# Kernel tuning notes

Hardware: AMD Instinct MI355X
Metric: run time of the kernel (lower is better)

Reference implementation:

```python
import jax, jax.numpy as jnp
import numpy as np

BN_EPS = 1e-5

# Binary activation with hardtanh STE semantics (forward: sign)
@jax.custom_vjp
def binary_act(x):
    return jnp.sign(x)

def _ba_fwd(x):
    return jnp.sign(x), x

def _ba_bwd(x, g):
    return (jnp.where(jnp.abs(x) > 1.0, 0.0, g),)

binary_act.defvjp(_ba_fwd, _ba_bwd)

# Binary weight quantizer (forward: sign, backward: identity STE)
@jax.custom_vjp
def binary_w(x):
    return jnp.sign(x)

def _bw_fwd(x):
    return jnp.sign(x), None

def _bw_bwd(_, g):
    return (g,)

binary_w.defvjp(_bw_fwd, _bw_bwd)


def setup_inputs() -> dict:
    key = jax.random.key(0)
    k1, k2, k3 = jax.random.split(key, 3)
    B, C_in, H, W_sp = 32, 256, 56, 56
    C_out, KH, KW = 256, 3, 3
    x = jax.random.normal(k1, (B, C_in, H, W_sp), dtype=jnp.float32)
    weight = jax.random.normal(k2, (C_out, C_in, KH, KW), dtype=jnp.float32) * 0.05
    bias = jax.random.normal(k3, (C_out,), dtype=jnp.float32) * 0.01
    gamma = jnp.ones((C_out,), dtype=jnp.float32)
    beta = jnp.zeros((C_out,), dtype=jnp.float32)
    return {"x": x, "weight": weight, "bias": bias, "gamma": gamma, "beta": beta}


def reference(x, weight, bias, gamma, beta):
    # --- activation binarization (A=2): sign ---
    xb = binary_act(x)
    # --- weight binarization (W=2): mean-center over in-channel dim, clamp, sign * alpha ---
    wc = weight - jnp.mean(weight, axis=1, keepdims=True)
    wc = jnp.clip(wc, -1.0, 1.0)
    alpha = jnp.mean(jnp.abs(wc), axis=(1, 2, 3), keepdims=True)  # per-output-channel scale
    wq = binary_w(wc) * alpha
    # --- conv2d, stride 1, padding 1 ---
    y = jax.lax.conv_general_dilated(
        xb, wq, window_strides=(1, 1), padding=((1, 1), (1, 1)),
        dimension_numbers=("NCHW", "OIHW", "NCHW"))
    y = y + bias[None, :, None, None]
    # --- BatchNorm2d (training-mode batch statistics, biased variance) ---
    mu = jnp.mean(y, axis=(0, 2, 3), keepdims=True)
    var = jnp.var(y, axis=(0, 2, 3), keepdims=True)
    y = (y - mu) * jax.lax.rsqrt(var + BN_EPS)
    y = y * gamma[None, :, None, None] + beta[None, :, None, None]
    # --- last_relu=1 ---
    y = jax.nn.relu(y)
    # --- last_bin=1 (A=2 -> binary activation) ---
    y = binary_act(y)
    return y
```

## Files before the change

kernel.cpp:

```cpp
#include <hip/hip_runtime.h>

typedef unsigned long long u64;
typedef int i32x4 __attribute__((ext_vector_type(4)));
typedef int i32x16 __attribute__((ext_vector_type(16)));
typedef short s16x8 __attribute__((ext_vector_type(8)));
typedef float f32x4 __attribute__((ext_vector_type(4)));

#define N_SP 3136
#define C_IN 256
#define C_OUT 256
#define BATCH 32
#define NBLK 1792
#define XROW 64
#define XPLANE (58 * XROW * 256)
#define XSIZE ((size_t)BATCH * XPLANE)
#define S16_OFF ((size_t)36 << 20)
#define S16_BYTES ((size_t)BATCH * C_OUT * N_SP * 2)

__global__ __launch_bounds__(256) void prep_weights(const float* __restrict__ w,
                                                    char* __restrict__ A_pack,
                                                    double* __restrict__ alpha) {
    const int o = blockIdx.x;
    const int i = threadIdx.x;
    const int lane = i & 63, wvid = i >> 6;
    __shared__ double part[4][9];
    __shared__ double part2[4];

    float wv[9];
    const float* wp = w + ((size_t)o * C_IN + i) * 9;
#pragma unroll
    for (int t = 0; t < 9; ++t) wv[t] = wp[t];

#pragma unroll
    for (int t = 0; t < 9; ++t) {
        double v = (double)wv[t];
#pragma unroll
        for (int off = 32; off > 0; off >>= 1) v += __shfl_down(v, off);
        if (lane == 0) part[wvid][t] = v;
    }
    __syncthreads();

    double asum = 0.0;
#pragma unroll
    for (int t = 0; t < 9; ++t) {
        double mean = (part[0][t] + part[1][t] + part[2][t] + part[3][t]) * (1.0 / 256.0);
        double wc = (double)wv[t] - mean;
        int idx16 = ((t * 8 + (i >> 5)) * 8 + (o >> 5)) * 64 + (((i >> 4) & 1) << 5) + (o & 31);
        A_pack[(size_t)idx16 * 16 + (i & 15)] = (char)(wc > 0.0 ? 1 : -1);
        double aw = fabs(wc);
        if (aw > 1.0) aw = 1.0;
        asum += aw;
    }
#pragma unroll
    for (int off = 32; off > 0; off >>= 1) asum += __shfl_down(asum, off);
    if (lane == 0) part2[wvid] = asum;
    __syncthreads();
    if (i == 0)
        alpha[o] = (part2[0] + part2[1] + part2[2] + part2[3]) * (1.0 / 2304.0);
}

__global__ __launch_bounds__(256) void sign_transpose(const float* __restrict__ x,
                                                      char* __restrict__ xsT) {
    const int sp0 = blockIdx.x * 64;
    const int b = blockIdx.y;
    const int lane = threadIdx.x & 63;
    const int wv = threadIdx.x >> 6;
    __shared__ char tile[64 * 272];

    {
        const int tidl = (blockIdx.y * 49 + blockIdx.x) * 256 + threadIdx.x;
        if (tidl < 294912) {
            const int bb = tidl / 9216;
            const int r = tidl - bb * 9216;
            int hp, wp, c16;
            if (r < 2048) {
                hp = (r >> 10) * 57;
                wp = (r >> 4) & 63;
                c16 = (r & 15) << 4;
            } else {
                int r2 = r - 2048;
                hp = 1 + (r2 >> 7);
                int q = r2 & 127;
                int wi = q >> 4;
                wp = (wi == 0) ? 0 : 56 + wi;
                c16 = (q & 15) << 4;
            }
            *(i32x4*)(xsT + (((size_t)(bb * 58 + hp) << 6) + wp) * 256 + c16) =
                (i32x4){0, 0, 0, 0};
        }
    }

    const float* xp = x + ((size_t)(b * 256 + (wv << 6))) * N_SP + sp0 + lane;
#pragma unroll
    for (int q = 0; q < 4; ++q) {
        unsigned d[4];
#pragma unroll
        for (int dd = 0; dd < 4; ++dd) {
            unsigned v = 0;
#pragma unroll
            for (int kk = 0; kk < 4; ++kk) {
                int ci_l = (q << 4) + (dd << 2) + kk;
                float xv = __builtin_nontemporal_load(xp + (size_t)ci_l * N_SP);
                v |= (unsigned)(xv > 0.0f ? 0x01u : 0xFFu) << (8 * kk);
            }
            d[dd] = v;
        }
        *(i32x4*)(tile + lane * 272 + (wv << 6) + (q << 4)) =
            (i32x4){(int)d[0], (int)d[1], (int)d[2], (int)d[3]};
    }
    __syncthreads();

    const int t = threadIdx.x;
#pragma unroll
    for (int j = 0; j < 4; ++j) {
        int sp_loc = (j << 4) + (t >> 4);
        int ci0 = (t & 15) << 4;
        i32x4 v = *(const i32x4*)(tile + sp_loc * 272 + ci0);
        int spg = sp0 + sp_loc;
        int h = spg / 56, w = spg - h * 56;
        size_t dst = (((size_t)(b * 58 + h + 1) << 6) + (w + 1)) * 256 + ci0;
        *(i32x4*)(xsT + dst) = v;
    }
}

__global__ __launch_bounds__(256, 3) void conv_mfma(const char* __restrict__ xsT,
                                                    const char* __restrict__ A_pack,
                                                    float* __restrict__ out,
                                                    short* __restrict__ s16,
                                                    int2* __restrict__ partials) {
    const int tid = threadIdx.x;
    const int lane = tid & 63;
    const int wv = tid >> 6;
    const int l31 = lane & 31, l5 = lane >> 5;
    const int blk = blockIdx.x;
    const int b = blk / 56;
    const int h0 = blk - b * 56;

    __shared__ char slab[3 * 58 * 272];

    {
        const char* src = xsT + ((size_t)(b * 58 + h0) << 6) * 256;
        for (int c = tid; c < 3 * 58 * 16; c += 256) {
            int dh = c / (58 * 16);
            int rem = c - dh * (58 * 16);
            int wp = rem >> 4, c16 = (rem & 15) << 4;
            *(i32x4*)(slab + (dh * 58 + wp) * 272 + c16) =
                *(const i32x4*)(src + (size_t)dh * (XROW * 256) + wp * 256 + c16);
        }
    }
    __syncthreads();

    i32x16 acc[2][2] = {};

    const char* apb = A_pack + ((size_t)(2 * wv * 64 + lane)) * 16;
    const char* sb0 = slab + l31 * 272 + l5 * 16;
    int w1_0 = 32 + l31;     if (w1_0 > 57) w1_0 = 57;
    int w1_1 = 33 + l31;     if (w1_1 > 57) w1_1 = 57;
    int w1_2 = 34 + l31;     if (w1_2 > 57) w1_2 = 57;
    const char* sb1_0 = slab + w1_0 * 272 + l5 * 16;
    const char* sb1_1 = slab + w1_1 * 272 + l5 * 16;
    const char* sb1_2 = slab + w1_2 * 272 + l5 * 16;

#pragma unroll
    for (int tap = 0; tap < 9; ++tap) {
        const int dh = tap / 3, dw = tap - 3 * (tap / 3);
        const char* sb1 = (dw == 0) ? sb1_0 : ((dw == 1) ? sb1_1 : sb1_2);
#pragma unroll
        for (int cib = 0; cib < 8; ++cib) {
            const int it = tap * 8 + cib;
            i32x4 a0 = *(const i32x4*)(apb + (size_t)it * 8192);
            i32x4 a1 = *(const i32x4*)(apb + (size_t)it * 8192 + 1024);
            i32x4 b0 = *(const i32x4*)(sb0 + (dh * 58 + dw) * 272 + cib * 32);
            i32x4 b1 = *(const i32x4*)(sb1 + dh * 58 * 272 + cib * 32);
            acc[0][0] = __builtin_amdgcn_mfma_i32_32x32x32_i8(a0, b0, acc[0][0], 0, 0, 0);
            acc[0][1] = __builtin_amdgcn_mfma_i32_32x32x32_i8(a0, b1, acc[0][1], 0, 0, 0);
            acc[1][0] = __builtin_amdgcn_mfma_i32_32x32x32_i8(a1, b0, acc[1][0], 0, 0, 0);
            acc[1][1] = __builtin_amdgcn_mfma_i32_32x32x32_i8(a1, b1, acc[1][1], 0, 0, 0);
        }
    }

    if (s16) {
        short* sb = s16 + ((size_t)(b * 256)) * N_SP + h0 * 56;
#pragma unroll
        for (int co_i = 0; co_i < 2; ++co_i) {
            const int co5 = 2 * wv + co_i;
#pragma unroll
            for (int nh = 0; nh < 2; ++nh) {
                const int w = nh * 32 + l31;
                if (w < 56) {
#pragma unroll
                    for (int reg = 0; reg < 16; ++reg) {
                        int corow = (reg & 3) + 8 * (reg >> 2) + 4 * l5;
                        __builtin_nontemporal_store(
                            (short)acc[co_i][nh][reg],
                            sb + (size_t)(co5 * 32 + corow) * N_SP + w);
                    }
                }
            }
        }
    } else {
        float* ob = out + ((size_t)(b * 256)) * N_SP + h0 * 56;
#pragma unroll
        for (int co_i = 0; co_i < 2; ++co_i) {
            const int co5 = 2 * wv + co_i;
#pragma unroll
            for (int nh = 0; nh < 2; ++nh) {
                const int w = nh * 32 + l31;
                if (w < 56) {
#pragma unroll
                    for (int reg = 0; reg < 16; ++reg) {
                        int corow = (reg & 3) + 8 * (reg >> 2) + 4 * l5;
                        __builtin_nontemporal_store(
                            (float)acc[co_i][nh][reg],
                            ob + (size_t)(co5 * 32 + corow) * N_SP + w);
                    }
                }
            }
        }
    }

    __syncthreads();
    int* sp_s = (int*)slab;
    int* sp_q = (int*)slab + 256;
#pragma unroll
    for (int co_i = 0; co_i < 2; ++co_i) {
#pragma unroll
        for (int reg = 0; reg < 16; ++reg) {
            int v0 = acc[co_i][0][reg];
            int v1 = (l31 < 24) ? acc[co_i][1][reg] : 0;
            int s = v0 + v1;
            unsigned q = (unsigned)(v0 * v0) + (unsigned)(v1 * v1);
#pragma unroll
            for (int off = 16; off > 0; off >>= 1) {
                s += __shfl_xor(s, off);
                q += (unsigned)__shfl_xor((int)q, off);
            }
            if (l31 == 0) {
                int corow = (reg & 3) + 8 * (reg >> 2) + 4 * l5;
                sp_s[(2 * wv + co_i) * 32 + corow] = s;
                sp_q[(2 * wv + co_i) * 32 + corow] = (int)q;
            }
        }
    }
    __syncthreads();
    {
        u64 v = (u64)(unsigned)sp_s[tid] | ((u64)(unsigned)sp_q[tid] << 32);
        __builtin_nontemporal_store(v, (u64*)(partials + (size_t)tid * NBLK + blk));
    }
}

__global__ __launch_bounds__(256) void stats_consts(const int2* __restrict__ partials,
                                                    const double* __restrict__ alpha,
                                                    const float* __restrict__ gamma,
                                                    const float* __restrict__ beta,
                                                    double* __restrict__ AB) {
    const int c = blockIdx.x;
    const int t = threadIdx.x;
    long long s1 = 0, s2 = 0;
    for (int blk = t; blk < NBLK; blk += 256) {
        int2 v = partials[(size_t)c * NBLK + blk];
        s1 += v.x;
        s2 += (long long)v.y;
    }
#pragma unroll
    for (int off = 32; off > 0; off >>= 1) {
        s1 += __shfl_down(s1, off);
        s2 += __shfl_down(s2, off);
    }
    __shared__ long long p1[4], p2[4];
    if ((t & 63) == 0) { p1[t >> 6] = s1; p2[t >> 6] = s2; }
    __syncthreads();
    if (t == 0) {
        double S1 = (double)(p1[0] + p1[1] + p1[2] + p1[3]);
        double S2 = (double)(p2[0] + p2[1] + p2[2] + p2[3]);
        const double N = (double)(BATCH * N_SP);
        double mu = S1 / N;
        double var = S2 / N - mu * mu;
        double a = alpha[c];
        double vy = a * a * var;
        double scale = (double)gamma[c] / sqrt(vy + 1e-5);
        double A = a * scale;
        double B = (double)beta[c] - A * mu;
        AB[c] = A;
        AB[C_OUT + c] = B;
    }
}

__global__ __launch_bounds__(256) void finalize(float* __restrict__ out,
                                                const double* __restrict__ AB) {
    const unsigned i4 = blockIdx.x * 256 + threadIdx.x;
    const unsigned e = i4 << 2;
    const int c = (int)((e / N_SP) & (C_OUT - 1));
    const double A = AB[c];
    const double B = AB[C_OUT + c];
    float4 v = ((float4*)out)[i4];
    v.x = (A * (double)v.x + B) > 0.0 ? 1.0f : 0.0f;
    v.y = (A * (double)v.y + B) > 0.0 ? 1.0f : 0.0f;
    v.z = (A * (double)v.z + B) > 0.0 ? 1.0f : 0.0f;
    v.w = (A * (double)v.w + B) > 0.0 ? 1.0f : 0.0f;
    ((float4*)out)[i4] = v;
}

__global__ __launch_bounds__(256) void finalize16(const short* __restrict__ S,
                                                  float* __restrict__ out,
                                                  const double* __restrict__ AB) {
    const unsigned t = blockIdx.x * 256 + threadIdx.x;
    const unsigned e = t << 3;
    const int c = (int)((e / N_SP) & (C_OUT - 1));
    const double A = AB[c];
    const double B = AB[C_OUT + c];
    s16x8 v = __builtin_nontemporal_load((const s16x8*)(S + e));
    f32x4 o0, o1;
    o0.x = (A * (double)v[0] + B) > 0.0 ? 1.0f : 0.0f;
    o0.y = (A * (double)v[1] + B) > 0.0 ? 1.0f : 0.0f;
    o0.z = (A * (double)v[2] + B) > 0.0 ? 1.0f : 0.0f;
    o0.w = (A * (double)v[3] + B) > 0.0 ? 1.0f : 0.0f;
    o1.x = (A * (double)v[4] + B) > 0.0 ? 1.0f : 0.0f;
    o1.y = (A * (double)v[5] + B) > 0.0 ? 1.0f : 0.0f;
    o1.z = (A * (double)v[6] + B) > 0.0 ? 1.0f : 0.0f;
    o1.w = (A * (double)v[7] + B) > 0.0 ? 1.0f : 0.0f;
    __builtin_nontemporal_store(o0, (f32x4*)(out + e));
    __builtin_nontemporal_store(o1, (f32x4*)(out + e + 4));
}

extern "C" void kernel_launch(void* const* d_in, const int* in_sizes, int n_in,
                              void* d_out, int out_size, void* d_ws, size_t ws_size,
                              hipStream_t stream) {
    const float* x      = (const float*)d_in[0];
    const float* weight = (const float*)d_in[1];
    const float* bias   = (const float*)d_in[2];   (void)bias;
    const float* gamma  = (const float*)d_in[3];
    const float* beta   = (const float*)d_in[4];
    float* out = (float*)d_out;

    char* ws = (char*)d_ws;
    double* alpha = (double*)(ws + 4096);
    double* AB    = (double*)(ws + 8192);
    char*   A_pack = (char*)(ws + 16384);
    int2*   partials = (int2*)(ws + (1 << 20));
    char*   xsT   = (char*)(ws + (5 << 20));
    const bool use16 = ws_size >= S16_OFF + S16_BYTES;
    short*  s16 = use16 ? (short*)(ws + S16_OFF) : (short*)0;

    prep_weights<<<C_OUT, 256, 0, stream>>>(weight, A_pack, alpha);
    sign_transpose<<<dim3(49, BATCH), 256, 0, stream>>>(x, xsT);
    conv_mfma<<<dim3(NBLK), 256, 0, stream>>>(xsT, A_pack, out, s16, partials);
    stats_consts<<<C_OUT, 256, 0, stream>>>(partials, alpha, gamma, beta, AB);
    if (use16)
        finalize16<<<12544, 256, 0, stream>>>(s16, out, AB);
    else
        finalize<<<(out_size / 4) / 256, 256, 0, stream>>>(out, AB);
}
```

Measured before the change: 319.0 us.

## Stage weight fragments into LDS via async global_load_lds with 3-deep prefetch

Weight fragments were previously loaded directly from global memory into registers in every MFMA iteration. They are now streamed into a per-wave 4-slot LDS ring using global_load_lds, issued three iterations ahead, with explicit vmcnt waits. The aim is to hide global load latency behind the MFMA work. Each wave only reads the slots it filled itself, so no block barrier is added. The cost is more LDS per block, hand-tuned waitcnt and scheduling barriers, and launch bounds lowered from 3 to 2 blocks per CU, which reduces occupancy.

```diff
diff --git a/kernel.cpp b/kernel.cpp
--- a/kernel.cpp
+++ b/kernel.cpp
@@ -123,7 +123,7 @@
     }
 }
 
-__global__ __launch_bounds__(256, 3) void conv_mfma(const char* __restrict__ xsT,
+__global__ __launch_bounds__(256, 2) void conv_mfma(const char* __restrict__ xsT,
                                                     const char* __restrict__ A_pack,
                                                     float* __restrict__ out,
                                                     short* __restrict__ s16,
@@ -137,6 +137,19 @@
     const int h0 = blk - b * 56;
 
     __shared__ char slab[3 * 58 * 272];
+    __shared__ i32x4 abuf[4][4][128];
+
+#define STAGE_A(IT)                                                              \
+    {                                                                            \
+        const char* g_ = A_pack + (size_t)(IT)*8192 + wv * 2048 + lane * 16;     \
+        char* l_ = (char*)&abuf[wv][(IT)&3][0];                                  \
+        __builtin_amdgcn_global_load_lds(                                        \
+            (const __attribute__((address_space(1))) unsigned*)g_,               \
+            (__attribute__((address_space(3))) unsigned*)l_, 16, 0, 0);          \
+        __builtin_amdgcn_global_load_lds(                                        \
+            (const __attribute__((address_space(1))) unsigned*)(g_ + 1024),      \
+            (__attribute__((address_space(3))) unsigned*)(l_ + 1024), 16, 0, 0); \
+    }
 
     {
         const char* src = xsT + ((size_t)(b * 58 + h0) << 6) * 256;
@@ -148,11 +161,13 @@
                 *(const i32x4*)(src + (size_t)dh * (XROW * 256) + wp * 256 + c16);
         }
     }
+
+    STAGE_A(0) STAGE_A(1) STAGE_A(2)
+
     __syncthreads();
 
     i32x16 acc[2][2] = {};
 
-    const char* apb = A_pack + ((size_t)(2 * wv * 64 + lane)) * 16;
     const char* sb0 = slab + l31 * 272 + l5 * 16;
     int w1_0 = 32 + l31;     if (w1_0 > 57) w1_0 = 57;
     int w1_1 = 33 + l31;     if (w1_1 > 57) w1_1 = 57;
@@ -160,24 +175,31 @@
     const char* sb1_0 = slab + w1_0 * 272 + l5 * 16;
     const char* sb1_1 = slab + w1_1 * 272 + l5 * 16;
     const char* sb1_2 = slab + w1_2 * 272 + l5 * 16;
-
-#pragma unroll
-    for (int tap = 0; tap < 9; ++tap) {
+    const char* ab = (const char*)&abuf[wv][0][0] + lane * 16;
+
+#pragma unroll
+    for (int it = 0; it < 72; ++it) {
+        const int tap = it >> 3, cib = it & 7;
         const int dh = tap / 3, dw = tap - 3 * (tap / 3);
+        __builtin_amdgcn_sched_barrier(0);
+        if (it + 3 < 72) { STAGE_A(it + 3) }
+        if (it <= 68)      asm volatile("s_waitcnt vmcnt(6)" ::: "memory");
+        else if (it == 69) asm volatile("s_waitcnt vmcnt(4)" ::: "memory");
+        else if (it == 70) asm volatile("s_waitcnt vmcnt(2)" ::: "memory");
+        else               asm volatile("s_waitcnt vmcnt(0)" ::: "memory");
+        __builtin_amdgcn_sched_barrier(0);
+        const char* ap_ = ab + (it & 3) * 2048;
+        i32x4 a0 = *(const i32x4*)(ap_);
+        i32x4 a1 = *(const i32x4*)(ap_ + 1024);
         const char* sb1 = (dw == 0) ? sb1_0 : ((dw == 1) ? sb1_1 : sb1_2);
-#pragma unroll
-        for (int cib = 0; cib < 8; ++cib) {
-            const int it = tap * 8 + cib;
-            i32x4 a0 = *(const i32x4*)(apb + (size_t)it * 8192);
-            i32x4 a1 = *(const i32x4*)(apb + (size_t)it * 8192 + 1024);
-            i32x4 b0 = *(const i32x4*)(sb0 + (dh * 58 + dw) * 272 + cib * 32);
-            i32x4 b1 = *(const i32x4*)(sb1 + dh * 58 * 272 + cib * 32);
-            acc[0][0] = __builtin_amdgcn_mfma_i32_32x32x32_i8(a0, b0, acc[0][0], 0, 0, 0);
-            acc[0][1] = __builtin_amdgcn_mfma_i32_32x32x32_i8(a0, b1, acc[0][1], 0, 0, 0);
-            acc[1][0] = __builtin_amdgcn_mfma_i32_32x32x32_i8(a1, b0, acc[1][0], 0, 0, 0);
-            acc[1][1] = __builtin_amdgcn_mfma_i32_32x32x32_i8(a1, b1, acc[1][1], 0, 0, 0);
-        }
-    }
+        i32x4 b0 = *(const i32x4*)(sb0 + (dh * 58 + dw) * 272 + cib * 32);
+        i32x4 b1 = *(const i32x4*)(sb1 + dh * 58 * 272 + cib * 32);
+        acc[0][0] = __builtin_amdgcn_mfma_i32_32x32x32_i8(a0, b0, acc[0][0], 0, 0, 0);
+        acc[0][1] = __builtin_amdgcn_mfma_i32_32x32x32_i8(a0, b1, acc[0][1], 0, 0, 0);
+        acc[1][0] = __builtin_amdgcn_mfma_i32_32x32x32_i8(a1, b0, acc[1][0], 0, 0, 0);
+        acc[1][1] = __builtin_amdgcn_mfma_i32_32x32x32_i8(a1, b1, acc[1][1], 0, 0, 0);
+    }
+#undef STAGE_A
 
     if (s16) {
         short* sb = s16 + ((size_t)(b * 256)) * N_SP + h0 * 56;
```

Result: slower. 331.3 us (+3.8%).

## Split conv output channels across 8 waves with 512-thread blocks

Applied to the files above, without the earlier changes.

The conv kernel now launches 512 threads per block, so each of 8 waves computes 32 output channels instead of 4 waves each computing 64. This halves per-wave accumulator registers and A-operand loads, with the aim of raising occupancy and spreading MFMA work across more waves. In exchange, each B fragment is read from shared memory by twice as many waves, and barrier costs per block grow. The epilogue stores and the statistics reduction are adjusted to match.

```diff
diff --git a/kernel.cpp b/kernel.cpp
--- a/kernel.cpp
+++ b/kernel.cpp
@@ -123,7 +123,7 @@
     }
 }
 
-__global__ __launch_bounds__(256, 3) void conv_mfma(const char* __restrict__ xsT,
+__global__ __launch_bounds__(512, 4) void conv_mfma(const char* __restrict__ xsT,
                                                     const char* __restrict__ A_pack,
                                                     float* __restrict__ out,
                                                     short* __restrict__ s16,
@@ -140,7 +140,7 @@
 
     {
         const char* src = xsT + ((size_t)(b * 58 + h0) << 6) * 256;
-        for (int c = tid; c < 3 * 58 * 16; c += 256) {
+        for (int c = tid; c < 3 * 58 * 16; c += 512) {
             int dh = c / (58 * 16);
             int rem = c - dh * (58 * 16);
             int wp = rem >> 4, c16 = (rem & 15) << 4;
@@ -150,9 +150,9 @@
     }
     __syncthreads();
 
-    i32x16 acc[2][2] = {};
-
-    const char* apb = A_pack + ((size_t)(2 * wv * 64 + lane)) * 16;
+    i32x16 acc[2] = {};
+
+    const char* apb = A_pack + (size_t)(wv * 1024) + lane * 16;
     const char* sb0 = slab + l31 * 272 + l5 * 16;
     int w1_0 = 32 + l31;     if (w1_0 > 57) w1_0 = 57;
     int w1_1 = 33 + l31;     if (w1_1 > 57) w1_1 = 57;
@@ -168,52 +168,41 @@
 #pragma unroll
         for (int cib = 0; cib < 8; ++cib) {
             const int it = tap * 8 + cib;
-            i32x4 a0 = *(const i32x4*)(apb + (size_t)it * 8192);
-            i32x4 a1 = *(const i32x4*)(apb + (size_t)it * 8192 + 1024);
+            i32x4 a = *(const i32x4*)(apb + (size_t)it * 8192);
             i32x4 b0 = *(const i32x4*)(sb0 + (dh * 58 + dw) * 272 + cib * 32);
             i32x4 b1 = *(const i32x4*)(sb1 + dh * 58 * 272 + cib * 32);
-            acc[0][0] = __builtin_amdgcn_mfma_i32_32x32x32_i8(a0, b0, acc[0][0], 0, 0, 0);
-            acc[0][1] = __builtin_amdgcn_mfma_i32_32x32x32_i8(a0, b1, acc[0][1], 0, 0, 0);
-            acc[1][0] = __builtin_amdgcn_mfma_i32_32x32x32_i8(a1, b0, acc[1][0], 0, 0, 0);
-            acc[1][1] = __builtin_amdgcn_mfma_i32_32x32x32_i8(a1, b1, acc[1][1], 0, 0, 0);
+            acc[0] = __builtin_amdgcn_mfma_i32_32x32x32_i8(a, b0, acc[0], 0, 0, 0);
+            acc[1] = __builtin_amdgcn_mfma_i32_32x32x32_i8(a, b1, acc[1], 0, 0, 0);
         }
     }
 
     if (s16) {
-        short* sb = s16 + ((size_t)(b * 256)) * N_SP + h0 * 56;
-#pragma unroll
-        for (int co_i = 0; co_i < 2; ++co_i) {
-            const int co5 = 2 * wv + co_i;
-#pragma unroll
-            for (int nh = 0; nh < 2; ++nh) {
-                const int w = nh * 32 + l31;
-                if (w < 56) {
-#pragma unroll
-                    for (int reg = 0; reg < 16; ++reg) {
-                        int corow = (reg & 3) + 8 * (reg >> 2) + 4 * l5;
-                        __builtin_nontemporal_store(
-                            (short)acc[co_i][nh][reg],
-                            sb + (size_t)(co5 * 32 + corow) * N_SP + w);
-                    }
+        short* sb = s16 + ((size_t)(b * 256 + wv * 32)) * N_SP + h0 * 56;
+#pragma unroll
+        for (int nh = 0; nh < 2; ++nh) {
+            const int w = nh * 32 + l31;
+            if (w < 56) {
+#pragma unroll
+                for (int reg = 0; reg < 16; ++reg) {
+                    int corow = (reg & 3) + 8 * (reg >> 2) + 4 * l5;
+                    __builtin_nontemporal_store(
+                        (short)acc[nh][reg],
+                        sb + (size_t)corow * N_SP + w);
                 }
             }
         }
     } else {
-        float* ob = out + ((size_t)(b * 256)) * N_SP + h0 * 56;
-#pragma unroll
-        for (int co_i = 0; co_i < 2; ++co_i) {
-            const int co5 = 2 * wv + co_i;
-#pragma unroll
-            for (int nh = 0; nh < 2; ++nh) {
-                const int w = nh * 32 + l31;
-                if (w < 56) {
-#pragma unroll
-                    for (int reg = 0; reg < 16; ++reg) {
-                        int corow = (reg & 3) + 8 * (reg >> 2) + 4 * l5;
-                        __builtin_nontemporal_store(
-                            (float)acc[co_i][nh][reg],
-                            ob + (size_t)(co5 * 32 + corow) * N_SP + w);
-                    }
+        float* ob = out + ((size_t)(b * 256 + wv * 32)) * N_SP + h0 * 56;
+#pragma unroll
+        for (int nh = 0; nh < 2; ++nh) {
+            const int w = nh * 32 + l31;
+            if (w < 56) {
+#pragma unroll
+                for (int reg = 0; reg < 16; ++reg) {
+                    int corow = (reg & 3) + 8 * (reg >> 2) + 4 * l5;
+                    __builtin_nontemporal_store(
+                        (float)acc[nh][reg],
+                        ob + (size_t)corow * N_SP + w);
                 }
             }
         }
@@ -223,27 +212,24 @@
     int* sp_s = (int*)slab;
     int* sp_q = (int*)slab + 256;
 #pragma unroll
-    for (int co_i = 0; co_i < 2; ++co_i) {
-#pragma unroll
-        for (int reg = 0; reg < 16; ++reg) {
-            int v0 = acc[co_i][0][reg];
-            int v1 = (l31 < 24) ? acc[co_i][1][reg] : 0;
-            int s = v0 + v1;
-            unsigned q = (unsigned)(v0 * v0) + (unsigned)(v1 * v1);
-#pragma unroll
-            for (int off = 16; off > 0; off >>= 1) {
-                s += __shfl_xor(s, off);
-                q += (unsigned)__shfl_xor((int)q, off);
-            }
-            if (l31 == 0) {
-                int corow = (reg & 3) + 8 * (reg >> 2) + 4 * l5;
-                sp_s[(2 * wv + co_i) * 32 + corow] = s;
-                sp_q[(2 * wv + co_i) * 32 + corow] = (int)q;
-            }
-        }
-    }
-    __syncthreads();
-    {
+    for (int reg = 0; reg < 16; ++reg) {
+        int v0 = acc[0][reg];
+        int v1 = (l31 < 24) ? acc[1][reg] : 0;
+        int s = v0 + v1;
+        unsigned q = (unsigned)(v0 * v0) + (unsigned)(v1 * v1);
+#pragma unroll
+        for (int off = 16; off > 0; off >>= 1) {
+            s += __shfl_xor(s, off);
+            q += (unsigned)__shfl_xor((int)q, off);
+        }
+        if (l31 == 0) {
+            int corow = (reg & 3) + 8 * (reg >> 2) + 4 * l5;
+            sp_s[wv * 32 + corow] = s;
+            sp_q[wv * 32 + corow] = (int)q;
+        }
+    }
+    __syncthreads();
+    if (tid < 256) {
         u64 v = (u64)(unsigned)sp_s[tid] | ((u64)(unsigned)sp_q[tid] << 32);
         __builtin_nontemporal_store(v, (u64*)(partials + (size_t)tid * NBLK + blk));
     }
@@ -344,7 +330,7 @@
 
     prep_weights<<<C_OUT, 256, 0, stream>>>(weight, A_pack, alpha);
     sign_transpose<<<dim3(49, BATCH), 256, 0, stream>>>(x, xsT);
-    conv_mfma<<<dim3(NBLK), 256, 0, stream>>>(xsT, A_pack, out, s16, partials);
+    conv_mfma<<<dim3(NBLK), 512, 0, stream>>>(xsT, A_pack, out, s16, partials);
     stats_consts<<<C_OUT, 256, 0, stream>>>(partials, alpha, gamma, beta, AB);
     if (use16)
         finalize16<<<12544, 256, 0, stream>>>(s16, out, AB);
```

Result: faster. 307.6 us (-3.6%).
